# Performance work log

Hardware: AMD Instinct MI355X
Metric: run time of the kernel (lower is better)

## Reference

```python
import jax, jax.numpy as jnp
import numpy as np

L, B, S, H = 13, 32, 128, 768   # encoder hidden states: layers, batch (hardcoded 32), seq, hidden
U = 32                          # num_gru_units
G = 2 * U                       # linear out dim / bidirectional GRU feature dim (64)
NL = 2                          # num_labels
EPS = 1e-3                      # keras LayerNormalization default epsilon


def setup_inputs() -> dict:
    key = jax.random.key(0)
    ks = jax.random.split(key, 10)
    def n(k, shape, scale=0.05):
        return (jax.random.normal(k, shape, jnp.float32) * scale).astype(jnp.float32)
    return {
        "xs": jax.random.normal(ks[0], (L, B, S, H), jnp.float32),
        "W_lin": n(ks[1], (H, G)),
        "b_lin": jnp.zeros((G,), jnp.float32),
        "ln_gamma": jnp.ones((G,), jnp.float32),
        "ln_beta": jnp.zeros((G,), jnp.float32),
        "Wk_f": n(ks[2], (G, 3 * U)),
        "Wr_f": n(ks[3], (U, 3 * U)),
        "b_f": jnp.zeros((2, 3 * U), jnp.float32),   # [input_bias, recurrent_bias] (reset_after=True)
        "Wk_b": n(ks[4], (G, 3 * U)),
        "Wr_b": n(ks[5], (U, 3 * U)),
        "b_b": jnp.zeros((2, 3 * U), jnp.float32),
        "W_cls": n(ks[6], (G, NL)),
        "b_cls": jnp.zeros((NL,), jnp.float32),
    }


def _layernorm(x, g, b):
    m = jnp.mean(x, axis=-1, keepdims=True)
    v = jnp.var(x, axis=-1, keepdims=True)
    return (x - m) * jax.lax.rsqrt(v + EPS) * g + b


def _gru_dir(seq, h0, Wk, Wr, bias):
    # Keras GRU v2 cell (reset_after=True). seq: [B,S,G], h0: [B,U]
    xp = jnp.einsum('bsg,gk->bsk', seq, Wk) + bias[0]  # [B,S,3U]
    def step(h, x_t):
        rec = h @ Wr + bias[1]                          # [B,3U]
        z = jax.nn.sigmoid(x_t[:, :U] + rec[:, :U])
        r = jax.nn.sigmoid(x_t[:, U:2 * U] + rec[:, U:2 * U])
        hh = jnp.tanh(x_t[:, 2 * U:] + r * rec[:, 2 * U:])
        hn = z * h + (1.0 - z) * hh
        return hn, hn
    hT, ys = jax.lax.scan(step, h0, jnp.swapaxes(xp, 0, 1))  # scan over time
    return jnp.swapaxes(ys, 0, 1), hT                        # [B,S,U], [B,U]


def reference(xs, W_lin, b_lin, ln_gamma, ln_beta,
              Wk_f, Wr_f, b_f, Wk_b, Wr_b, b_b, W_cls, b_cls):
    # _forward: loop over the 13 encoder hidden-state layers; the bidirectional
    # GRU output feeds back as a residual into the next layer's linear output.
    # Dropout layers are treated as identity (deterministic reference), under
    # which the 100-pass MC average equals a single pass.
    seq = jnp.zeros((B, S, G), xs.dtype)  # initial 'sequence' of zeros
    h1 = jnp.zeros((B, U), xs.dtype)      # initial_state=None -> zeros in keras
    h2 = jnp.zeros((B, U), xs.dtype)
    for i in range(L):
        x = _layernorm(xs[i] @ W_lin + b_lin + seq, ln_gamma, ln_beta)  # [B,S,G]
        out_f, h1 = _gru_dir(x, h1, Wk_f, Wr_f, b_f)
        out_b, h2 = _gru_dir(x[:, ::-1], h2, Wk_b, Wr_b, b_b)
        seq = jnp.concatenate([out_f, out_b[:, ::-1]], axis=-1)         # [B,S,2U]
    # tf.stack([h1,h2], -1) -> [B,U,2]; reshape [32,-1] interleaves fwd/bwd units
    hcat = jnp.stack([h1, h2], axis=-1).reshape(B, -1)                  # [B,2U]
    return jax.nn.softmax(hcat @ W_cls + b_cls, axis=-1)                # [B,NL]
```

## Files before the change

### kernel.cpp

```cpp
#include <hip/hip_runtime.h>
#include <hip/hip_fp16.h>

#define L_ 13
#define B_ 32
#define S_ 128
#define H_ 768
#define NU 32
#define GG 64
#define TU 96
#define LN_EPS 1e-3f
#define SEQ_ST 68
#define XT_ST 129
#define WK_ST 100
#define XPH_ST 100
#define K1f 1.4426950408889634f
#define K2f 2.8853900817779268f

#define DPP_X1  0xB1
#define DPP_X2  0x4E
#define DPP_X7  0x141
#define DPP_X15 0x140

typedef float v2f __attribute__((ext_vector_type(2)));
typedef _Float16 h2t __attribute__((ext_vector_type(2)));
typedef unsigned int uv2 __attribute__((ext_vector_type(2)));

union F4H8 { float4 f4; __half2 hh[4]; h2t h[4]; };
union FH2  { float f; __half2 hh; h2t h; };
union F2H2 { float2 f2; __half2 hh[2]; };

__device__ __forceinline__ void pkfma(v2f& a, v2f x, v2f w) {
    asm("v_pk_fma_f32 %0, %1, %2, %0" : "+v"(a) : "v"(x), "v"(w));
}
template <int CTRL>
__device__ __forceinline__ float dppf(float x) {
    return __int_as_float(__builtin_amdgcn_update_dpp(
        0, __float_as_int(x), CTRL, 0xF, 0xF, true));
}
__device__ __forceinline__ float pairsum16(float x) {
#if __has_builtin(__builtin_amdgcn_permlane16_swap)
    uv2 s = __builtin_amdgcn_permlane16_swap(
        __float_as_uint(x), __float_as_uint(x), false, false);
    return __uint_as_float(s.x) + __uint_as_float(s.y);
#else
    return x + __shfl_xor(x, 16);
#endif
}

__global__ __launch_bounds__(256) void lin_kernel(
    const float* __restrict__ xs, const float* __restrict__ Wl,
    const float* __restrict__ bl, __half* __restrict__ lin)
{
    __shared__ float sA[64][68];
    __shared__ float sW[64][68];
    const int t = threadIdx.x;
    const size_t row0 = (size_t)blockIdx.x * 64;
    const int r4 = (t >> 4) << 2;
    const int c4 = (t & 15) << 2;

    float acc[4][4];
    #pragma unroll
    for (int i = 0; i < 4; ++i)
        #pragma unroll
        for (int j = 0; j < 4; ++j) acc[i][j] = 0.f;

    for (int kt = 0; kt < H_; kt += 64) {
        #pragma unroll
        for (int p = 0; p < 4; ++p) {
            int idx = t + 256 * p;
            int r = idx >> 4, cc = (idx & 15) << 2;
            *(float4*)&sA[r][cc] = *(const float4*)&xs[(row0 + r) * H_ + kt + cc];
            *(float4*)&sW[r][cc] = *(const float4*)&Wl[(size_t)(kt + r) * GG + cc];
        }
        __syncthreads();
        #pragma unroll 8
        for (int k = 0; k < 64; ++k) {
            float a0 = sA[r4 + 0][k], a1 = sA[r4 + 1][k], a2 = sA[r4 + 2][k], a3 = sA[r4 + 3][k];
            float4 w = *(const float4*)&sW[k][c4];
            acc[0][0] += a0 * w.x; acc[0][1] += a0 * w.y; acc[0][2] += a0 * w.z; acc[0][3] += a0 * w.w;
            acc[1][0] += a1 * w.x; acc[1][1] += a1 * w.y; acc[1][2] += a1 * w.z; acc[1][3] += a1 * w.w;
            acc[2][0] += a2 * w.x; acc[2][1] += a2 * w.y; acc[2][2] += a2 * w.z; acc[2][3] += a2 * w.w;
            acc[3][0] += a3 * w.x; acc[3][1] += a3 * w.y; acc[3][2] += a3 * w.z; acc[3][3] += a3 * w.w;
        }
        __syncthreads();
    }
    float4 bv = *(const float4*)&bl[c4];
    #pragma unroll
    for (int i = 0; i < 4; ++i) {
        F2H2 u;
        u.hh[0] = __floats2half2_rn(acc[i][0] + bv.x, acc[i][1] + bv.y);
        u.hh[1] = __floats2half2_rn(acc[i][2] + bv.z, acc[i][3] + bv.w);
        *(float2*)&lin[(row0 + r4 + i) * GG + c4] = u.f2;
    }
}

__global__ __launch_bounds__(512) void chain_kernel(
    const __half* __restrict__ lin_all,
    const float* __restrict__ Wr_f, const float* __restrict__ b_f,
    const float* __restrict__ Wr_b, const float* __restrict__ b_b,
    const float* __restrict__ Wk_f, const float* __restrict__ Wk_b,
    const float* __restrict__ ln_g, const float* __restrict__ ln_b,
    const float* __restrict__ W_cls, const float* __restrict__ b_cls,
    float* __restrict__ out)
{
    extern __shared__ float sm[];
    float*   seqb = sm;
    __half2* xt2  = (__half2*)(sm + 8704);
    __half2* wk2  = (__half2*)(sm + 8704 + 4128);
    __half*  xph  = (__half*)(sm + 8704 + 4128 + 6400);
    float*   hbf  = sm + 8704 + 4128 + 6400 + 12800;
    float*   hbb  = hbf + NU;

    const int b = blockIdx.x;
    const int t = threadIdx.x;
    const int wave = t >> 6;
    const int lane = t & 63;
    const int v16 = lane & 15;
    const int b4 = (lane >> 4) & 1;
    const int b5 = (lane >> 5) & 1;
    const int ud = v16 + 16 * b5;

    for (int i = t; i < S_ * SEQ_ST; i += 512) seqb[i] = 0.f;
    for (int i = t; i < 2 * 32 * 96; i += 512) {
        const int d = i / 3072, rem = i - d * 3072, k2 = rem / 96, c = rem - k2 * 96;
        const float* W = d ? Wk_b : Wk_f;
        const float sc = (c >= 64) ? K2f : K1f;
        wk2[(d * 32 + k2) * WK_ST + c] =
            __floats2half2_rn(W[(2 * k2) * TU + c] * sc, W[(2 * k2 + 1) * TU + c] * sc);
    }

    v2f wz[8], wr_[8], wh[8];
    float h_store = 0.f, h_dot = 0.f, rbz2 = 0.f, rbr2 = 0.f, rbh2 = 0.f;
    if (wave < 2) {
        const float* Wr   = wave ? Wr_b : Wr_f;
        const float* bias = wave ? b_b  : b_f;
        const int ex[8] = {0, 2, 7, 5, 15, 13, 8, 10};
        const int ey[8] = {1, 3, 6, 4, 14, 12, 9, 11};
        const int BB = 16 * b4;
        #pragma unroll
        for (int m = 0; m < 8; ++m) {
            const int jx = BB + (v16 ^ ex[m]), jy = BB + (v16 ^ ey[m]);
            wz[m]  = v2f{ K1f * Wr[jx * TU + ud],          K1f * Wr[jy * TU + ud] };
            wr_[m] = v2f{ K1f * Wr[jx * TU + NU + ud],     K1f * Wr[jy * TU + NU + ud] };
            wh[m]  = v2f{ K2f * Wr[jx * TU + 2 * NU + ud], K2f * Wr[jy * TU + 2 * NU + ud] };
        }
        rbz2 = 0.5f * K1f * bias[TU + ud];
        rbr2 = 0.5f * K1f * bias[TU + NU + ud];
        rbh2 = 0.5f * K2f * bias[TU + 2 * NU + ud];
    }

    const int g8 = t >> 3;
    const int c8 = (t & 7) << 3;
    const int rgrp = t & 31;
    const int cg = t >> 5;
    const int dsel = cg >> 3;
    const int cc = (cg & 7) * 12;
    const float* bias0 = dsel ? b_b : b_f;
    const __half2* wkd = wk2 + dsel * 32 * WK_ST;
    __half* xpd = xph + dsel * (S_ * XPH_ST);
    float bsc[12];
    #pragma unroll
    for (int m = 0; m < 12; ++m)
        bsc[m] = bias0[cc + m] * ((cc + m >= 64) ? K2f : K1f);

    __syncthreads();

    for (int l = 0; l < L_; ++l) {
        const __half* linb = lin_all + (size_t)(l * B_ + b) * S_ * GG;

        #pragma unroll
        for (int p = 0; p < 2; ++p) {
            const int r = g8 + 64 * p;
            F4H8 lu; lu.f4 = *(const float4*)&linb[(size_t)r * GG + c8];
            float4 s0 = *(const float4*)&seqb[r * SEQ_ST + c8];
            float4 s1 = *(const float4*)&seqb[r * SEQ_ST + c8 + 4];
            float2 l0 = __half22float2(lu.hh[0]);
            float2 l1 = __half22float2(lu.hh[1]);
            float2 l2 = __half22float2(lu.hh[2]);
            float2 l3 = __half22float2(lu.hh[3]);
            float v[8];
            v[0] = l0.x + s0.x; v[1] = l0.y + s0.y; v[2] = l1.x + s0.z; v[3] = l1.y + s0.w;
            v[4] = l2.x + s1.x; v[5] = l2.y + s1.y; v[6] = l3.x + s1.z; v[7] = l3.y + s1.w;
            float s = 0.f;
            #pragma unroll
            for (int j = 0; j < 8; ++j) s += v[j];
            #pragma unroll
            for (int off = 1; off < 8; off <<= 1) s += __shfl_xor(s, off);
            const float mean = s * 0.015625f;
            float q = 0.f;
            float d[8];
            #pragma unroll
            for (int j = 0; j < 8; ++j) { d[j] = v[j] - mean; q += d[j] * d[j]; }
            #pragma unroll
            for (int off = 1; off < 8; off <<= 1) q += __shfl_xor(q, off);
            const float rstd = rsqrtf(q * 0.015625f + LN_EPS);
            float4 g0 = *(const float4*)&ln_g[c8];
            float4 g1 = *(const float4*)&ln_g[c8 + 4];
            float4 b0 = *(const float4*)&ln_b[c8];
            float4 b1 = *(const float4*)&ln_b[c8 + 4];
            float x[8];
            x[0] = d[0] * rstd * g0.x + b0.x; x[1] = d[1] * rstd * g0.y + b0.y;
            x[2] = d[2] * rstd * g0.z + b0.z; x[3] = d[3] * rstd * g0.w + b0.w;
            x[4] = d[4] * rstd * g1.x + b1.x; x[5] = d[5] * rstd * g1.y + b1.y;
            x[6] = d[6] * rstd * g1.z + b1.z; x[7] = d[7] * rstd * g1.w + b1.w;
            #pragma unroll
            for (int j = 0; j < 4; ++j)
                xt2[(c8 / 2 + j) * XT_ST + r] = __floats2half2_rn(x[2 * j], x[2 * j + 1]);
        }
        __syncthreads();

        {
            float acc[4][12];
            #pragma unroll
            for (int m = 0; m < 12; ++m) {
                acc[0][m] = bsc[m]; acc[1][m] = bsc[m]; acc[2][m] = bsc[m]; acc[3][m] = bsc[m];
            }
            #pragma unroll 4
            for (int k2 = 0; k2 < 32; ++k2) {
                FH2 x0, x1, x2, x3;
                x0.hh = xt2[k2 * XT_ST + rgrp];
                x1.hh = xt2[k2 * XT_ST + rgrp + 32];
                x2.hh = xt2[k2 * XT_ST + rgrp + 64];
                x3.hh = xt2[k2 * XT_ST + rgrp + 96];
                F4H8 wa, wb, wc;
                wa.f4 = *(const float4*)&wkd[k2 * WK_ST + cc];
                wb.f4 = *(const float4*)&wkd[k2 * WK_ST + cc + 4];
                wc.f4 = *(const float4*)&wkd[k2 * WK_ST + cc + 8];
                #pragma unroll
                for (int m = 0; m < 4; ++m) {
                    acc[0][m]     = __builtin_amdgcn_fdot2(x0.h, wa.h[m], acc[0][m],     false);
                    acc[1][m]     = __builtin_amdgcn_fdot2(x1.h, wa.h[m], acc[1][m],     false);
                    acc[2][m]     = __builtin_amdgcn_fdot2(x2.h, wa.h[m], acc[2][m],     false);
                    acc[3][m]     = __builtin_amdgcn_fdot2(x3.h, wa.h[m], acc[3][m],     false);
                    acc[0][m + 4] = __builtin_amdgcn_fdot2(x0.h, wb.h[m], acc[0][m + 4], false);
                    acc[1][m + 4] = __builtin_amdgcn_fdot2(x1.h, wb.h[m], acc[1][m + 4], false);
                    acc[2][m + 4] = __builtin_amdgcn_fdot2(x2.h, wb.h[m], acc[2][m + 4], false);
                    acc[3][m + 4] = __builtin_amdgcn_fdot2(x3.h, wb.h[m], acc[3][m + 4], false);
                    acc[0][m + 8] = __builtin_amdgcn_fdot2(x0.h, wc.h[m], acc[0][m + 8], false);
                    acc[1][m + 8] = __builtin_amdgcn_fdot2(x1.h, wc.h[m], acc[1][m + 8], false);
                    acc[2][m + 8] = __builtin_amdgcn_fdot2(x2.h, wc.h[m], acc[2][m + 8], false);
                    acc[3][m + 8] = __builtin_amdgcn_fdot2(x3.h, wc.h[m], acc[3][m + 8], false);
                }
            }
            #pragma unroll
            for (int i = 0; i < 4; ++i) {
                const int r = rgrp + 32 * i;
                __half2* dst = (__half2*)&xpd[r * XPH_ST + cc];
                #pragma unroll
                for (int j = 0; j < 6; ++j)
                    dst[j] = __floats2half2_rn(acc[i][2 * j], acc[i][2 * j + 1]);
            }
        }
        __syncthreads();

        if (wave < 2) {
            const int dir = wave;
            const __half* xp = xph + dir * (S_ * XPH_ST);
            float* sq = seqb + dir * NU + (lane & 31);
            const int stp = dir ? -1 : 1;
            int s = dir ? (S_ - 1) : 0;
            const bool wl = (lane < 32);
            const bool fix = (b4 != b5);
            float xz = (float)xp[s * XPH_ST + ud];
            float xr = (float)xp[s * XPH_ST + 32 + ud];
            float xh = (float)xp[s * XPH_ST + 64 + ud];
            for (int st = 0; st < S_; ++st) {
                float nz = 0.f, nr = 0.f, nh = 0.f;
                if (st < S_ - 1) {
                    const int sn = s + stp;
                    nz = (float)xp[sn * XPH_ST + ud];
                    nr = (float)xp[sn * XPH_ST + 32 + ud];
                    nh = (float)xp[sn * XPH_ST + 64 + ud];
                }
                v2f ro[8];
                ro[0].x = h_store;                ro[0].y = dppf<DPP_X1>(h_store);
                ro[1].x = dppf<DPP_X2>(ro[0].x);  ro[1].y = dppf<DPP_X2>(ro[0].y);
                ro[2].x = dppf<DPP_X7>(ro[0].x);  ro[2].y = dppf<DPP_X7>(ro[0].y);
                ro[3].x = dppf<DPP_X7>(ro[1].x);  ro[3].y = dppf<DPP_X7>(ro[1].y);
                ro[4].x = dppf<DPP_X15>(ro[0].x); ro[4].y = dppf<DPP_X15>(ro[0].y);
                ro[5].x = dppf<DPP_X15>(ro[1].x); ro[5].y = dppf<DPP_X15>(ro[1].y);
                ro[6].x = dppf<DPP_X15>(ro[2].x); ro[6].y = dppf<DPP_X15>(ro[2].y);
                ro[7].x = dppf<DPP_X15>(ro[3].x); ro[7].y = dppf<DPP_X15>(ro[3].y);

                v2f aza = v2f{0.5f * xz + rbz2, 0.f}, azb = v2f{0.f, 0.f};
                v2f ara = v2f{0.5f * xr + rbr2, 0.f}, arb = v2f{0.f, 0.f};
                v2f aha = v2f{rbh2, 0.f},             ahb = v2f{0.f, 0.f};
                #pragma unroll
                for (int m = 0; m < 4; ++m) {
                    pkfma(aza, ro[m], wz[m]);      pkfma(azb, ro[m + 4], wz[m + 4]);
                    pkfma(ara, ro[m], wr_[m]);     pkfma(arb, ro[m + 4], wr_[m + 4]);
                    pkfma(aha, ro[m], wh[m]);      pkfma(ahb, ro[m + 4], wh[m + 4]);
                }
                v2f azs = aza + azb, ars = ara + arb, ahs = aha + ahb;
                const float pz = pairsum16(azs.x + azs.y);
                const float pr = pairsum16(ars.x + ars.y);
                const float ph = pairsum16(ahs.x + ahs.y);

                const float z  = __builtin_amdgcn_rcpf(1.0f + __builtin_amdgcn_exp2f(-pz));
                const float r  = __builtin_amdgcn_rcpf(1.0f + __builtin_amdgcn_exp2f(-pr));
                const float tt = xh + r * ph;
                const float et = __builtin_amdgcn_exp2f(-tt);
                const float hh = (1.0f - et) * __builtin_amdgcn_rcpf(1.0f + et);
                const float hn_raw = hh + z * (h_dot - hh);
                h_dot = hn_raw;
                uv2 s32 = __builtin_amdgcn_permlane32_swap(
                    __float_as_uint(hn_raw), __float_as_uint(hn_raw), false, false);
                const float v32 = wl ? __uint_as_float(s32.y) : __uint_as_float(s32.x);
                h_store = fix ? v32 : hn_raw;
                if (wl) sq[s * SEQ_ST] = h_store;
                s += stp; xz = nz; xr = nr; xh = nh;
            }
        }
        __syncthreads();
    }

    if (wave < 2 && lane < 32) (wave ? hbb : hbf)[lane & 31] = h_store;
    __syncthreads();
    if (t == 0) {
        float l0 = b_cls[0], l1 = b_cls[1];
        for (int j = 0; j < NU; ++j) {
            const float hf = hbf[j], hk = hbb[j];
            l0 += hf * W_cls[4 * j]     + hk * W_cls[4 * j + 2];
            l1 += hf * W_cls[4 * j + 1] + hk * W_cls[4 * j + 3];
        }
        const float m = fmaxf(l0, l1);
        const float e0 = __expf(l0 - m), e1 = __expf(l1 - m);
        const float inv = 1.0f / (e0 + e1);
        out[b * 2 + 0] = e0 * inv;
        out[b * 2 + 1] = e1 * inv;
    }
}

extern "C" void kernel_launch(void* const* d_in, const int* in_sizes, int n_in,
                              void* d_out, int out_size, void* d_ws, size_t ws_size,
                              hipStream_t stream) {
    const float* xs    = (const float*)d_in[0];
    const float* W_lin = (const float*)d_in[1];
    const float* b_lin = (const float*)d_in[2];
    const float* ln_g  = (const float*)d_in[3];
    const float* ln_b  = (const float*)d_in[4];
    const float* Wk_f  = (const float*)d_in[5];
    const float* Wr_f  = (const float*)d_in[6];
    const float* b_f   = (const float*)d_in[7];
    const float* Wk_b  = (const float*)d_in[8];
    const float* Wr_b  = (const float*)d_in[9];
    const float* b_b   = (const float*)d_in[10];
    const float* W_cls = (const float*)d_in[11];
    const float* b_cls = (const float*)d_in[12];
    float* out = (float*)d_out;

    __half* lin_all = (__half*)d_ws;

    const int smem = (8704 + 4128 + 6400 + 12800 + 64) * (int)sizeof(float);
    (void)hipFuncSetAttribute((const void*)chain_kernel,
                              hipFuncAttributeMaxDynamicSharedMemorySize, smem);

    lin_kernel<<<(L_ * B_ * S_) / 64, 256, 0, stream>>>(xs, W_lin, b_lin, lin_all);

    chain_kernel<<<B_, 512, smem, stream>>>(
        lin_all, Wr_f, b_f, Wr_b, b_b, Wk_f, Wk_b, ln_g, ln_b, W_cls, b_cls, out);
}
```

Baseline: 598.2 us.

## Fuse linear GEMM into chain kernel with per-layer atomic counters for overlap

Merges the input projection kernel into the recurrent chain kernel as extra producer blocks. Each producer computes one (layer, batch) tile of 128 rows using fp16 dot2 instructions and increments a per-layer counter. Chain blocks poll that counter before each layer, so the recurrent chain can start on layer 0 while later layers are still being projected. This overlaps the memory-bound GEMM with the latency-bound recurrence. In exchange it adds fp16 rounding of the input activations, a spin-wait that relies on producer blocks being co-resident with the chain blocks, and a large dynamic shared allocation for every producer block, which limits occupancy.

```diff
diff --git a/kernel.cpp b/kernel.cpp
--- a/kernel.cpp
+++ b/kernel.cpp
@@ -46,56 +46,18 @@
     return x + __shfl_xor(x, 16);
 #endif
 }
-
-__global__ __launch_bounds__(256) void lin_kernel(
+__device__ __forceinline__ void poll_ge_dev(unsigned* p, unsigned tgt) {
+    int gd = 0;
+    while (__hip_atomic_load(p, __ATOMIC_ACQUIRE, __HIP_MEMORY_SCOPE_AGENT) < tgt) {
+        __builtin_amdgcn_s_sleep(2);
+        if (++gd > (1 << 22)) break;
+    }
+}
+
+__global__ __launch_bounds__(512) void fused_kernel(
     const float* __restrict__ xs, const float* __restrict__ Wl,
-    const float* __restrict__ bl, __half* __restrict__ lin)
-{
-    __shared__ float sA[64][68];
-    __shared__ float sW[64][68];
-    const int t = threadIdx.x;
-    const size_t row0 = (size_t)blockIdx.x * 64;
-    const int r4 = (t >> 4) << 2;
-    const int c4 = (t & 15) << 2;
-
-    float acc[4][4];
-    #pragma unroll
-    for (int i = 0; i < 4; ++i)
-        #pragma unroll
-        for (int j = 0; j < 4; ++j) acc[i][j] = 0.f;
-
-    for (int kt = 0; kt < H_; kt += 64) {
-        #pragma unroll
-        for (int p = 0; p < 4; ++p) {
-            int idx = t + 256 * p;
-            int r = idx >> 4, cc = (idx & 15) << 2;
-            *(float4*)&sA[r][cc] = *(const float4*)&xs[(row0 + r) * H_ + kt + cc];
-            *(float4*)&sW[r][cc] = *(const float4*)&Wl[(size_t)(kt + r) * GG + cc];
-        }
-        __syncthreads();
-        #pragma unroll 8
-        for (int k = 0; k < 64; ++k) {
-            float a0 = sA[r4 + 0][k], a1 = sA[r4 + 1][k], a2 = sA[r4 + 2][k], a3 = sA[r4 + 3][k];
-            float4 w = *(const float4*)&sW[k][c4];
-            acc[0][0] += a0 * w.x; acc[0][1] += a0 * w.y; acc[0][2] += a0 * w.z; acc[0][3] += a0 * w.w;
-            acc[1][0] += a1 * w.x; acc[1][1] += a1 * w.y; acc[1][2] += a1 * w.z; acc[1][3] += a1 * w.w;
-            acc[2][0] += a2 * w.x; acc[2][1] += a2 * w.y; acc[2][2] += a2 * w.z; acc[2][3] += a2 * w.w;
-            acc[3][0] += a3 * w.x; acc[3][1] += a3 * w.y; acc[3][2] += a3 * w.z; acc[3][3] += a3 * w.w;
-        }
-        __syncthreads();
-    }
-    float4 bv = *(const float4*)&bl[c4];
-    #pragma unroll
-    for (int i = 0; i < 4; ++i) {
-        F2H2 u;
-        u.hh[0] = __floats2half2_rn(acc[i][0] + bv.x, acc[i][1] + bv.y);
-        u.hh[1] = __floats2half2_rn(acc[i][2] + bv.z, acc[i][3] + bv.w);
-        *(float2*)&lin[(row0 + r4 + i) * GG + c4] = u.f2;
-    }
-}
-
-__global__ __launch_bounds__(512) void chain_kernel(
-    const __half* __restrict__ lin_all,
+    const float* __restrict__ bl,
+    __half* __restrict__ lin_all, unsigned* __restrict__ lincnt,
     const float* __restrict__ Wr_f, const float* __restrict__ b_f,
     const float* __restrict__ Wr_b, const float* __restrict__ b_b,
     const float* __restrict__ Wk_f, const float* __restrict__ Wk_b,
@@ -104,6 +66,80 @@
     float* __restrict__ out)
 {
     extern __shared__ float sm[];
+    const int bid = blockIdx.x;
+    const int t = threadIdx.x;
+
+    if (bid >= B_) {
+        const int tix = bid - B_;
+        const int l = tix >> 5;
+        const int bb = tix & 31;
+        const size_t row0 = (size_t)(l * B_ + bb) * S_;
+        __half2* sA2 = (__half2*)sm;
+        __half2* sW2 = (__half2*)(sm + 32 * 132);
+
+        const int rgrp = t & 31;
+        const int cg = t >> 5;
+        const int c0 = cg * 4;
+
+        float acc[4][4];
+        #pragma unroll
+        for (int i = 0; i < 4; ++i)
+            #pragma unroll
+            for (int j = 0; j < 4; ++j) acc[i][j] = 0.f;
+
+        for (int kt = 0; kt < H_; kt += 64) {
+            #pragma unroll
+            for (int i = 0; i < 4; ++i) {
+                const int idx = t + 512 * i;
+                const int r = idx >> 4, kq = idx & 15;
+                float4 a = *(const float4*)&xs[(row0 + r) * H_ + kt + kq * 4];
+                sA2[(2 * kq) * 132 + r]     = __floats2half2_rn(a.x, a.y);
+                sA2[(2 * kq + 1) * 132 + r] = __floats2half2_rn(a.z, a.w);
+            }
+            {
+                const int k2 = t >> 4, c4 = (t & 15) * 4;
+                float4 w0 = *(const float4*)&Wl[(size_t)(kt + 2 * k2) * GG + c4];
+                float4 w1 = *(const float4*)&Wl[(size_t)(kt + 2 * k2 + 1) * GG + c4];
+                sW2[k2 * 68 + c4 + 0] = __floats2half2_rn(w0.x, w1.x);
+                sW2[k2 * 68 + c4 + 1] = __floats2half2_rn(w0.y, w1.y);
+                sW2[k2 * 68 + c4 + 2] = __floats2half2_rn(w0.z, w1.z);
+                sW2[k2 * 68 + c4 + 3] = __floats2half2_rn(w0.w, w1.w);
+            }
+            __syncthreads();
+            #pragma unroll 4
+            for (int k2 = 0; k2 < 32; ++k2) {
+                FH2 x0, x1, x2, x3;
+                x0.hh = sA2[k2 * 132 + rgrp];
+                x1.hh = sA2[k2 * 132 + rgrp + 32];
+                x2.hh = sA2[k2 * 132 + rgrp + 64];
+                x3.hh = sA2[k2 * 132 + rgrp + 96];
+                F4H8 w; w.f4 = *(const float4*)&sW2[k2 * 68 + c0];
+                #pragma unroll
+                for (int m = 0; m < 4; ++m) {
+                    acc[0][m] = __builtin_amdgcn_fdot2(x0.h, w.h[m], acc[0][m], false);
+                    acc[1][m] = __builtin_amdgcn_fdot2(x1.h, w.h[m], acc[1][m], false);
+                    acc[2][m] = __builtin_amdgcn_fdot2(x2.h, w.h[m], acc[2][m], false);
+                    acc[3][m] = __builtin_amdgcn_fdot2(x3.h, w.h[m], acc[3][m], false);
+                }
+            }
+            __syncthreads();
+        }
+        const float4 bv = *(const float4*)&bl[c0];
+        #pragma unroll
+        for (int i = 0; i < 4; ++i) {
+            const int r = rgrp + 32 * i;
+            F2H2 u;
+            u.hh[0] = __floats2half2_rn(acc[i][0] + bv.x, acc[i][1] + bv.y);
+            u.hh[1] = __floats2half2_rn(acc[i][2] + bv.z, acc[i][3] + bv.w);
+            *(float2*)&lin_all[(row0 + r) * GG + c0] = u.f2;
+        }
+        __threadfence();
+        __syncthreads();
+        if (t == 0)
+            __hip_atomic_fetch_add(&lincnt[l], 1u, __ATOMIC_RELEASE, __HIP_MEMORY_SCOPE_AGENT);
+        return;
+    }
+
     float*   seqb = sm;
     __half2* xt2  = (__half2*)(sm + 8704);
     __half2* wk2  = (__half2*)(sm + 8704 + 4128);
@@ -111,8 +147,7 @@
     float*   hbf  = sm + 8704 + 4128 + 6400 + 12800;
     float*   hbb  = hbf + NU;
 
-    const int b = blockIdx.x;
-    const int t = threadIdx.x;
+    const int b = bid;
     const int wave = t >> 6;
     const int lane = t & 63;
     const int v16 = lane & 15;
@@ -167,6 +202,9 @@
 
     for (int l = 0; l < L_; ++l) {
         const __half* linb = lin_all + (size_t)(l * B_ + b) * S_ * GG;
+
+        if (t == 0) poll_ge_dev(&lincnt[l], 32u);
+        __syncthreads();
 
         #pragma unroll
         for (int p = 0; p < 2; ++p) {
@@ -349,14 +387,17 @@
     const float* b_cls = (const float*)d_in[12];
     float* out = (float*)d_out;
 
-    __half* lin_all = (__half*)d_ws;
+    char* ws = (char*)d_ws;
+    __half* lin_all = (__half*)ws;
+    unsigned* lincnt = (unsigned*)(ws + 6815744);
+
+    hipMemsetAsync(lincnt, 0, 64, stream);
 
     const int smem = (8704 + 4128 + 6400 + 12800 + 64) * (int)sizeof(float);
-    (void)hipFuncSetAttribute((const void*)chain_kernel,
+    (void)hipFuncSetAttribute((const void*)fused_kernel,
                               hipFuncAttributeMaxDynamicSharedMemorySize, smem);
 
-    lin_kernel<<<(L_ * B_ * S_) / 64, 256, 0, stream>>>(xs, W_lin, b_lin, lin_all);
-
-    chain_kernel<<<B_, 512, smem, stream>>>(
-        lin_all, Wr_f, b_f, Wr_b, b_b, Wk_f, Wk_b, ln_g, ln_b, W_cls, b_cls, out);
-}
+    fused_kernel<<<B_ + L_ * B_, 512, smem, stream>>>(
+        xs, W_lin, b_lin, lin_all, lincnt,
+        Wr_f, b_f, Wr_b, b_b, Wk_f, Wk_b, ln_g, ln_b, W_cls, b_cls, out);
+}
```

After: 613.5 us. 2.6% more time.
